# Kernel tuning notes

Hardware: AMD Instinct MI355X
Metric: run time of the kernel (lower is better)

Reference implementation:

```python
import jax, jax.numpy as jnp
import numpy as np

N = 10000      # nodes
E = 160000     # edges
C = 72         # hidden dim = 18 * mul (mul=4)
A = 16         # node_attr dim (16x0e)
L = 3          # layers
O = 64         # output dim (64x0e)
B = 16         # graphs in batch
IN_DIM = 18    # irreps_node_input dim
SH = 9         # spherical harmonics dim, lmax=2
FC = 100       # radial MLP hidden (fc_neurons=[1,100])
MAX_RADIUS = 2.0
NUM_NEIGHBORS = 16.0
NUM_NODES = 625.0


def sph_harm_l2(d):
    # component-normalized real spherical harmonics up to l=2 on unit vectors d [E,3]
    x, y, z = d[:, 0], d[:, 1], d[:, 2]
    s3, s5, s15 = 3.0 ** 0.5, 5.0 ** 0.5, 15.0 ** 0.5
    return jnp.stack([
        jnp.ones_like(x),
        s3 * x, s3 * y, s3 * z,
        s15 * x * y, s15 * y * z, (s5 / 2.0) * (3.0 * z * z - 1.0),
        s15 * x * z, (s15 / 2.0) * (x * x - y * y),
    ], axis=1)  # [E, 9]


def setup_inputs() -> dict:
    key = jax.random.key(0)
    ks = jax.random.split(key, 16)
    pos = jax.random.normal(ks[0], (N, 3), dtype=jnp.float32)
    node_attr = jax.random.normal(ks[1], (N, A), dtype=jnp.float32)
    batch = jnp.sort(jax.random.randint(ks[2], (N,), 0, B))
    edge_src = jax.random.randint(ks[3], (E,), 0, N)
    edge_dst = jax.random.randint(ks[4], (E,), 0, N)
    W_in = jax.random.normal(ks[5], (IN_DIM, C), dtype=jnp.float32) / np.sqrt(IN_DIM)
    W_tp = jax.random.normal(ks[6], (L, SH, C, C), dtype=jnp.float32) / np.sqrt(C)
    W_self = jax.random.normal(ks[7], (L, C, C), dtype=jnp.float32) / np.sqrt(C)
    W_attr = jax.random.normal(ks[8], (L, A, C), dtype=jnp.float32) / np.sqrt(A)
    fc1_w = jax.random.normal(ks[9], (L, 1, FC), dtype=jnp.float32)
    fc1_b = jnp.zeros((L, FC), dtype=jnp.float32)
    fc2_w = jax.random.normal(ks[10], (L, FC, SH), dtype=jnp.float32) / np.sqrt(FC)
    W_out = jax.random.normal(ks[11], (C, O), dtype=jnp.float32) / np.sqrt(C)
    return {"pos": pos, "node_attr": node_attr, "batch": batch,
            "edge_src": edge_src, "edge_dst": edge_dst,
            "W_in": W_in, "W_tp": W_tp, "W_self": W_self, "W_attr": W_attr,
            "fc1_w": fc1_w, "fc1_b": fc1_b, "fc2_w": fc2_w, "W_out": W_out}


def reference(pos, node_attr, batch, edge_src, edge_dst,
              W_in, W_tp, W_self, W_attr, fc1_w, fc1_b, fc2_w, W_out):
    n = pos.shape[0]
    # edge geometry
    rvec = pos[edge_src] - pos[edge_dst]                      # [E,3]
    r = jnp.linalg.norm(rvec, axis=1, keepdims=True)          # [E,1]
    dvec = rvec / jnp.maximum(r, 1e-9)
    sh = sph_harm_l2(dvec)                                    # [E,9]
    # single cosine radial basis with cutoff at max_radius (number_of_basis=1)
    t = r / MAX_RADIUS
    emb = jnp.where(t < 1.0, jnp.cos(0.5 * jnp.pi * t), 0.0)  # [E,1]
    # node inputs: fixed one-hot on the scalar channel, embedded to hidden dim
    onehot = jnp.zeros((IN_DIM,), dtype=pos.dtype).at[0].set(1.0)
    h = jnp.broadcast_to((onehot @ W_in)[None, :], (n, C))    # [N,C]
    for l in range(L):
        # radial MLP -> per-edge, per-SH-path weights
        u = jax.nn.silu(emb @ fc1_w[l] + fc1_b[l]) @ fc2_w[l]  # [E,9]
        path = u * sh                                          # [E,9]
        hs = h[edge_src]                                       # [E,C]
        m = jnp.zeros_like(hs)
        for s in range(SH):  # fixed small set of tensor-product paths
            m = m + path[:, s:s + 1] * (hs @ W_tp[l, s])       # [E,C]
        agg = jax.ops.segment_sum(m, edge_dst, num_segments=n) / np.sqrt(NUM_NEIGHBORS)
        h = jax.nn.gelu(agg + h @ W_self[l] + node_attr @ W_attr[l])
    out_nodes = h @ W_out                                      # [N,O]
    pooled = jax.ops.segment_sum(out_nodes, batch, num_segments=B)
    return pooled / np.sqrt(NUM_NODES)                         # [B,O]
```

## Files before the change

kernel.cpp:

```cpp
#include <hip/hip_runtime.h>
#include <math.h>

#define NN 10000
#define NE 160000
#define CC 72
#define AA 16
#define LL 3
#define OO 64
#define NBATCH 16
#define SH 9
#define FCN 100
#define KK (SH*CC)
#define KA 736
#define KP 768
#define KG 96
#define NT 5
#define PSTRIDE 12
#define NB 1024
#define EMAX 176

typedef __attribute__((ext_vector_type(8))) short bf16x8;
typedef __attribute__((ext_vector_type(4))) float f32x4;

static __device__ __forceinline__ float gelu_tanh(float x) {
    float x3 = x * x * x;
    float inner = 0.7978845608028654f * (x + 0.044715f * x3);
    return 0.5f * x * (1.0f + tanhf(inner));
}
static __device__ __forceinline__ unsigned short f2bf(float x) {
    unsigned int u = __float_as_uint(x);
    u += 0x7FFFu + ((u >> 16) & 1u);
    return (unsigned short)(u >> 16);
}
static __device__ __forceinline__ float bf2f(unsigned short u) {
    return __uint_as_float((unsigned int)u << 16);
}
static __device__ __forceinline__ unsigned int pack2bf(float lo, float hi) {
    return (unsigned int)f2bf(lo) | ((unsigned int)f2bf(hi) << 16);
}

__global__ void k_zero(int* __restrict__ cnt) {
    int i = blockIdx.x * blockDim.x + threadIdx.x;
    if (i < NN) cnt[i] = 0;
}

#define GB_HIST 625
#define GB_UTAB 13
#define GB_WCAT 180
#define GB_INIT 704
#define GB_PREP (GB_HIST + GB_UTAB + GB_WCAT + GB_INIT)

__global__ __launch_bounds__(256) void k_prep(
        const float* __restrict__ pos, const int* __restrict__ esrc,
        const int* __restrict__ edst, int* __restrict__ cnt,
        const float* __restrict__ fc1w, const float* __restrict__ fc1b,
        const float* __restrict__ fc2w, float* __restrict__ U,
        const float* __restrict__ Wtp, const float* __restrict__ Wself,
        const float* __restrict__ Wattr, unsigned short* __restrict__ Wb,
        const float* __restrict__ W_in, unsigned short* __restrict__ h0) {
    int bb = blockIdx.x, t = threadIdx.x;
    if (bb < GB_HIST) {
        int e = bb * 256 + t;
        if (e < NE) {
            int s = esrc[e], d = edst[e];
            float dx = pos[3 * s] - pos[3 * d];
            float dy = pos[3 * s + 1] - pos[3 * d + 1];
            float dz = pos[3 * s + 2] - pos[3 * d + 2];
            float r = sqrtf(dx * dx + dy * dy + dz * dz);
            if (r * 0.5f < 1.0f) atomicAdd(&cnt[d], 1);
        }
        return;
    }
    bb -= GB_HIST;
    if (bb < GB_UTAB) {
        int i = bb * 256 + t;
        if (i < LL * (NB + 1)) {
            int l = i / (NB + 1), b = i - l * (NB + 1);
            float emb = cosf(1.5707963267948966f * ((float)b / (float)NB));
            float u[SH];
#pragma unroll
            for (int q = 0; q < SH; ++q) u[q] = 0.f;
            const float* w1 = &fc1w[l * FCN];
            const float* b1 = &fc1b[l * FCN];
            const float* w2 = &fc2w[l * FCN * SH];
            for (int f = 0; f < FCN; ++f) {
                float a = emb * w1[f] + b1[f];
                float si = a / (1.0f + expf(-a));
#pragma unroll
                for (int q = 0; q < SH; ++q) u[q] += si * w2[f * SH + q];
            }
            float* ud = &U[(size_t)i * 12];
#pragma unroll
            for (int q = 0; q < SH; ++q) ud[q] = u[q];
            ud[9] = 0.f; ud[10] = 0.f; ud[11] = 0.f;
        }
        return;
    }
    bb -= GB_UTAB;
    if (bb < GB_WCAT) {
        int i0 = (bb * 256 + t) * 4;
#pragma unroll
        for (int u = 0; u < 4; ++u) {
            int i = i0 + u;
            int l = i / (NT * KG * 128);
            int rem = i - l * (NT * KG * 128);
            int nt = rem / (KG * 128); rem -= nt * (KG * 128);
            int kg = rem / 128; int e = rem - kg * 128;
            int n = nt * 16 + (e >> 3);
            int k = kg * 8 + (e & 7);
            float v = 0.f;
            if (n < CC && k < KA) {
                if (k < KK)            v = 0.25f * Wtp[(size_t)l * KK * CC + k * CC + n];
                else if (k < KK + CC)  v = Wself[(size_t)l * CC * CC + (k - KK) * CC + n];
                else                   v = Wattr[(size_t)l * AA * CC + (k - KK - CC) * CC + n];
            }
            Wb[i] = f2bf(v);
        }
        return;
    }
    bb -= GB_WCAT;
    {
        int i0 = (bb * 256 + t) * 4;
#pragma unroll
        for (int u = 0; u < 4; ++u) {
            int i = i0 + u;
            if (i < NN * CC) h0[i] = f2bf(W_in[i % CC]);
        }
    }
}

__global__ void k_scan(const int* __restrict__ cnt, int* __restrict__ off,
                       int* __restrict__ cur, float* __restrict__ hp) {
    __shared__ int sa[256], sb[256];
    const int PER = 40;
    int t = threadIdx.x;
    int base = t * PER;
    int loc[PER];
    int run = 0;
#pragma unroll
    for (int i = 0; i < PER; ++i) {
        int idx = base + i;
        int v = (idx < NN) ? cnt[idx] : 0;
        loc[i] = run;
        run += v;
    }
    sa[t] = run;
    __syncthreads();
    int* in = sa; int* out = sb;
    for (int o = 1; o < 256; o <<= 1) {
        int v = in[t];
        if (t >= o) v += in[t - o];
        out[t] = v;
        __syncthreads();
        int* tmp = in; in = out; out = tmp;
    }
    int ebase = (t > 0) ? in[t - 1] : 0;
#pragma unroll
    for (int i = 0; i < PER; ++i) {
        int idx = base + i;
        if (idx <= NN) {
            int v = ebase + loc[i];
            off[idx] = v;
            if (idx < NN) cur[idx] = v;
        }
    }
    for (int i = t; i < NBATCH * CC; i += 256) hp[i] = 0.f;
}

__global__ __launch_bounds__(256) void k_scatter3(const float* __restrict__ pos,
                                                  const int* __restrict__ esrc,
                                                  const int* __restrict__ edst,
                                                  int* __restrict__ cur,
                                                  int* __restrict__ src_s,
                                                  const float* __restrict__ U,
                                                  float* __restrict__ path) {
    int e = blockIdx.x * blockDim.x + threadIdx.x;
    if (e >= NE) return;
    int s = esrc[e], d = edst[e];
    float dx = pos[3 * s] - pos[3 * d];
    float dy = pos[3 * s + 1] - pos[3 * d + 1];
    float dz = pos[3 * s + 2] - pos[3 * d + 2];
    float r = sqrtf(dx * dx + dy * dy + dz * dz);
    if (r * 0.5f >= 1.0f) return;
    int slot = atomicAdd(&cur[d], 1);
    src_s[slot] = s;

    float inv = 1.0f / fmaxf(r, 1e-9f);
    float x = dx * inv, y = dy * inv, z = dz * inv;
    const float s3 = 1.7320508075688772f;
    const float s5 = 2.23606797749979f;
    const float s15 = 3.872983346207417f;
    float sh[SH];
    sh[0] = 1.0f;
    sh[1] = s3 * x;
    sh[2] = s3 * y;
    sh[3] = s3 * z;
    sh[4] = s15 * x * y;
    sh[5] = s15 * y * z;
    sh[6] = 0.5f * s5 * (3.0f * z * z - 1.0f);
    sh[7] = s15 * x * z;
    sh[8] = 0.5f * s15 * (x * x - y * y);

    float fb = r * 0.5f * (float)NB;
    int b0 = (int)fb;
    float fr = fb - (float)b0;

#pragma unroll
    for (int l = 0; l < LL; ++l) {
        const float* t0 = &U[((size_t)l * (NB + 1) + b0) * 12];
        float4 a0 = *(const float4*)(t0 + 0);
        float4 a1 = *(const float4*)(t0 + 4);
        float  a2 = t0[8];
        float4 c0 = *(const float4*)(t0 + 12);
        float4 c1 = *(const float4*)(t0 + 16);
        float  c2 = t0[20];
        float u0 = a0.x + fr * (c0.x - a0.x);
        float u1 = a0.y + fr * (c0.y - a0.y);
        float u2 = a0.z + fr * (c0.z - a0.z);
        float u3 = a0.w + fr * (c0.w - a0.w);
        float u4 = a1.x + fr * (c1.x - a1.x);
        float u5 = a1.y + fr * (c1.y - a1.y);
        float u6 = a1.z + fr * (c1.z - a1.z);
        float u7 = a1.w + fr * (c1.w - a1.w);
        float u8 = a2   + fr * (c2   - a2);
        float* pd = &path[((size_t)l * NE + slot) * PSTRIDE];
        *(float4*)(pd + 0) = make_float4(u0 * sh[0], u1 * sh[1], u2 * sh[2], u3 * sh[3]);
        *(float4*)(pd + 4) = make_float4(u4 * sh[4], u5 * sh[5], u6 * sh[6], u7 * sh[7]);
        *(float4*)(pd + 8) = make_float4(u8 * sh[8], 0.f, 0.f, 0.f);
    }
}

__global__ __launch_bounds__(1024, 8) void k_layer(
        const unsigned short* __restrict__ h,
        const float* __restrict__ attr,
        const float* __restrict__ path_l,
        const int* __restrict__ src_s,
        const int* __restrict__ off,
        const unsigned short* __restrict__ Wb,
        unsigned short* __restrict__ hout) {
    __shared__ float Plds[EMAX * PSTRIDE];
    __shared__ unsigned short Alds[KG * 128];
    int t = threadIdx.x, w = t >> 6, lane = t & 63;
    int n0 = blockIdx.x * 16;
    int d = n0 + w;
    int b0 = off[n0], e0 = off[n0 + 16];
    int db = off[d], de = off[d + 1];

    bool act = lane < 36;
    int c2 = 2 * lane;
    float a1[SH], a2[SH];
#pragma unroll
    for (int q = 0; q < SH; ++q) { a1[q] = 0.f; a2[q] = 0.f; }

    for (int base = b0; base < e0; base += EMAX) {
        int nE = min(EMAX, e0 - base);
        const float4* p4 = (const float4*)(path_l + (size_t)base * PSTRIDE);
        for (int idx = t; idx < nE * 3; idx += 1024)
            *(float4*)&Plds[idx * 4] = p4[idx];
        __syncthreads();
        int lb = db > base ? db : base;
        int le = de < base + nE ? de : base + nE;
        for (int i = lb; i < le; i += 4) {
            int m = le - i;
            unsigned int hv[4];
#pragma unroll
            for (int j = 0; j < 4; ++j) {
                if (j < m && act) {
                    int s = src_s[i + j];
                    hv[j] = *(const unsigned int*)&h[(size_t)s * CC + c2];
                }
            }
#pragma unroll
            for (int j = 0; j < 4; ++j) {
                if (j < m) {
                    const float* p = &Plds[(i + j - base) * PSTRIDE];
                    float4 p0 = *(const float4*)p;
                    float4 p1 = *(const float4*)(p + 4);
                    float p8 = p[8];
                    float lo = act ? bf2f((unsigned short)(hv[j] & 0xffffu)) : 0.f;
                    float hi = act ? bf2f((unsigned short)(hv[j] >> 16)) : 0.f;
                    a1[0] += p0.x * lo; a2[0] += p0.x * hi;
                    a1[1] += p0.y * lo; a2[1] += p0.y * hi;
                    a1[2] += p0.z * lo; a2[2] += p0.z * hi;
                    a1[3] += p0.w * lo; a2[3] += p0.w * hi;
                    a1[4] += p1.x * lo; a2[4] += p1.x * hi;
                    a1[5] += p1.y * lo; a2[5] += p1.y * hi;
                    a1[6] += p1.z * lo; a2[6] += p1.z * hi;
                    a1[7] += p1.w * lo; a2[7] += p1.w * hi;
                    a1[8] += p8 * lo;   a2[8] += p8 * hi;
                }
            }
        }
        __syncthreads();
    }

    if (act) {
        int kgo = lane >> 2, kjo = 2 * (lane & 3);
        int hb = w * 8 + kjo;
#pragma unroll
        for (int q = 0; q < SH; ++q)
            *(unsigned int*)&Alds[(9 * q + kgo) * 128 + hb] = pack2bf(a1[q], a2[q]);
        *(unsigned int*)&Alds[(81 + kgo) * 128 + hb] =
            *(const unsigned int*)&h[(size_t)d * CC + c2];
        if (lane < 8)
            *(unsigned int*)&Alds[(90 + kgo) * 128 + hb] =
                pack2bf(attr[(size_t)d * AA + c2], attr[(size_t)d * AA + c2 + 1]);
    }
    if (lane < 16)
        *(unsigned int*)&Alds[(92 + (lane >> 2)) * 128 + w * 8 + 2 * (lane & 3)] = 0u;
    __syncthreads();

    if (w < NT) {
        const unsigned short* Ab = Alds + (lane & 15) * 8;
        const unsigned short* Bb = Wb + ((size_t)w * KG) * 128 + (lane & 15) * 8;
        f32x4 acc = (f32x4){0.f, 0.f, 0.f, 0.f};
#pragma unroll
        for (int s = 0; s < 24; ++s) {
            int kg = s * 4 + (lane >> 4);
            bf16x8 af = *(const bf16x8*)(Ab + (size_t)kg * 128);
            bf16x8 bq = *(const bf16x8*)(Bb + (size_t)kg * 128);
            acc = __builtin_amdgcn_mfma_f32_16x16x32_bf16(af, bq, acc, 0, 0, 0);
        }
        int cb = lane & 15, rb = (lane >> 4) * 4;
        int row = n0 + rb, col = w * 16 + cb;
        if (col < CC) {
#pragma unroll
            for (int j = 0; j < 4; ++j)
                hout[(size_t)(row + j) * CC + col] = f2bf(gelu_tanh(acc[j]));
        }
    }
}

__global__ __launch_bounds__(256) void k_pool(const unsigned short* __restrict__ h,
                                              const int* __restrict__ batch,
                                              float* __restrict__ hp) {
    __shared__ float sp[NBATCH * CC];
    int t = threadIdx.x;
    for (int i = t; i < NBATCH * CC; i += 256) sp[i] = 0.f;
    __syncthreads();
    int n0 = blockIdx.x * 16;
    for (int i = t; i < 16 * CC; i += 256) {
        int nl = i / CC, c = i - nl * CC;
        int n = n0 + nl;
        if (n < NN) atomicAdd(&sp[batch[n] * CC + c], bf2f(h[(size_t)n * CC + c]));
    }
    __syncthreads();
    for (int i = t; i < NBATCH * CC; i += 256) {
        float v = sp[i];
        if (v != 0.f) atomicAdd(&hp[i], v);
    }
}

__global__ __launch_bounds__(1024) void k_outmm(const float* __restrict__ hp,
                                                const float* __restrict__ Wout,
                                                float* __restrict__ out) {
    __shared__ float hs[NBATCH * CC];
    int t = threadIdx.x;
    for (int i = t; i < NBATCH * CC; i += 1024) hs[i] = hp[i];
    __syncthreads();
    int b = t >> 6, o = t & 63;
    float acc = 0.f;
#pragma unroll 8
    for (int c = 0; c < CC; ++c) acc += hs[b * CC + c] * Wout[c * OO + o];
    out[t] = acc * (1.0f / 25.0f);
}

extern "C" void kernel_launch(void* const* d_in, const int* in_sizes, int n_in,
                              void* d_out, int out_size, void* d_ws, size_t ws_size,
                              hipStream_t stream) {
    const float* pos       = (const float*)d_in[0];
    const float* node_attr = (const float*)d_in[1];
    const int*   batch     = (const int*)d_in[2];
    const int*   esrc      = (const int*)d_in[3];
    const int*   edst      = (const int*)d_in[4];
    const float* W_in      = (const float*)d_in[5];
    const float* W_tp      = (const float*)d_in[6];
    const float* W_self    = (const float*)d_in[7];
    const float* W_attr    = (const float*)d_in[8];
    const float* fc1w      = (const float*)d_in[9];
    const float* fc1b      = (const float*)d_in[10];
    const float* fc2w      = (const float*)d_in[11];
    const float* W_out     = (const float*)d_in[12];
    float* out = (float*)d_out;

    char* p = (char*)d_ws;
    auto alloc = [&](size_t bytes) -> void* {
        void* r = (void*)p;
        p += (bytes + 255) & ~(size_t)255;
        return r;
    };
    int*   cnt   = (int*)alloc((size_t)NN * 4);
    int*   cur   = (int*)alloc((size_t)NN * 4);
    float* hp    = (float*)alloc((size_t)NBATCH * CC * 4);
    int*   off   = (int*)alloc((size_t)(NN + 1) * 4);
    int*   src_s = (int*)alloc((size_t)NE * 4);
    float* path  = (float*)alloc((size_t)LL * NE * PSTRIDE * 4);
    float* U     = (float*)alloc((size_t)LL * (NB + 1) * 12 * 4);
    unsigned short* Wb = (unsigned short*)alloc((size_t)LL * NT * KG * 128 * 2);
    unsigned short* h0 = (unsigned short*)alloc((size_t)NN * CC * 2);
    unsigned short* h1 = (unsigned short*)alloc((size_t)NN * CC * 2);

    k_zero<<<(NN + 255) / 256, 256, 0, stream>>>(cnt);
    k_prep<<<GB_PREP, 256, 0, stream>>>(pos, esrc, edst, cnt, fc1w, fc1b, fc2w, U,
                                        W_tp, W_self, W_attr, Wb, W_in, h0);
    k_scan<<<1, 256, 0, stream>>>(cnt, off, cur, hp);
    k_scatter3<<<(NE + 255) / 256, 256, 0, stream>>>(pos, esrc, edst, cur, src_s, U, path);

    const unsigned short* hin = h0;
    unsigned short* hout = h1;
    for (int l = 0; l < LL; ++l) {
        k_layer<<<NN / 16, 1024, 0, stream>>>(hin, node_attr,
                                              path + (size_t)l * NE * PSTRIDE, src_s, off,
                                              Wb + (size_t)l * NT * KG * 128, hout);
        const unsigned short* tmp = hin; hin = hout; hout = (unsigned short*)tmp;
    }
    k_pool<<<(NN + 15) / 16, 256, 0, stream>>>(hin, batch, hp);
    k_outmm<<<1, 1024, 0, stream>>>(hp, W_out, out);
}
```

Measured before the change: 139.0 us.

## Store per-edge path weights in bf16 and read them directly without LDS staging

Per-edge path coefficients are now packed as bf16 (16-element stride) instead of fp32 (12-element stride), halving the write traffic in the scatter kernel and the read traffic in each layer. The layer kernel drops the block-wide LDS staging of path values and its two __syncthreads per chunk. Each wave instead loads its own edges' path values straight from global memory alongside the gathered h values. This removes barrier stalls and the shared-memory footprint, at the cost of lower precision in the path weights and redundant global loads issued per lane.

```diff
diff --git a/kernel.cpp b/kernel.cpp
--- a/kernel.cpp
+++ b/kernel.cpp
@@ -15,9 +15,8 @@
 #define KP 768
 #define KG 96
 #define NT 5
-#define PSTRIDE 12
+#define PSU 16
 #define NB 1024
-#define EMAX 176
 
 typedef __attribute__((ext_vector_type(8))) short bf16x8;
 typedef __attribute__((ext_vector_type(4))) float f32x4;
@@ -37,6 +36,12 @@
 }
 static __device__ __forceinline__ unsigned int pack2bf(float lo, float hi) {
     return (unsigned int)f2bf(lo) | ((unsigned int)f2bf(hi) << 16);
+}
+static __device__ __forceinline__ float bfLo(unsigned int u) {
+    return __uint_as_float(u << 16);
+}
+static __device__ __forceinline__ float bfHi(unsigned int u) {
+    return __uint_as_float(u & 0xffff0000u);
 }
 
 __global__ void k_zero(int* __restrict__ cnt) {
@@ -173,7 +178,7 @@
                                                   int* __restrict__ cur,
                                                   int* __restrict__ src_s,
                                                   const float* __restrict__ U,
-                                                  float* __restrict__ path) {
+                                                  unsigned short* __restrict__ path) {
     int e = blockIdx.x * blockDim.x + threadIdx.x;
     if (e >= NE) return;
     int s = esrc[e], d = edst[e];
@@ -214,36 +219,37 @@
         float4 c0 = *(const float4*)(t0 + 12);
         float4 c1 = *(const float4*)(t0 + 16);
         float  c2 = t0[20];
-        float u0 = a0.x + fr * (c0.x - a0.x);
-        float u1 = a0.y + fr * (c0.y - a0.y);
-        float u2 = a0.z + fr * (c0.z - a0.z);
-        float u3 = a0.w + fr * (c0.w - a0.w);
-        float u4 = a1.x + fr * (c1.x - a1.x);
-        float u5 = a1.y + fr * (c1.y - a1.y);
-        float u6 = a1.z + fr * (c1.z - a1.z);
-        float u7 = a1.w + fr * (c1.w - a1.w);
-        float u8 = a2   + fr * (c2   - a2);
-        float* pd = &path[((size_t)l * NE + slot) * PSTRIDE];
-        *(float4*)(pd + 0) = make_float4(u0 * sh[0], u1 * sh[1], u2 * sh[2], u3 * sh[3]);
-        *(float4*)(pd + 4) = make_float4(u4 * sh[4], u5 * sh[5], u6 * sh[6], u7 * sh[7]);
-        *(float4*)(pd + 8) = make_float4(u8 * sh[8], 0.f, 0.f, 0.f);
+        float u0 = (a0.x + fr * (c0.x - a0.x)) * sh[0];
+        float u1 = (a0.y + fr * (c0.y - a0.y)) * sh[1];
+        float u2 = (a0.z + fr * (c0.z - a0.z)) * sh[2];
+        float u3 = (a0.w + fr * (c0.w - a0.w)) * sh[3];
+        float u4 = (a1.x + fr * (c1.x - a1.x)) * sh[4];
+        float u5 = (a1.y + fr * (c1.y - a1.y)) * sh[5];
+        float u6 = (a1.z + fr * (c1.z - a1.z)) * sh[6];
+        float u7 = (a1.w + fr * (c1.w - a1.w)) * sh[7];
+        float u8 = (a2   + fr * (c2   - a2))   * sh[8];
+        unsigned short* pd = &path[((size_t)l * NE + slot) * PSU];
+        uint4 w0, w1;
+        w0.x = pack2bf(u0, u1); w0.y = pack2bf(u2, u3);
+        w0.z = pack2bf(u4, u5); w0.w = pack2bf(u6, u7);
+        w1.x = pack2bf(u8, 0.f); w1.y = 0u; w1.z = 0u; w1.w = 0u;
+        *(uint4*)pd = w0;
+        *(uint4*)(pd + 8) = w1;
     }
 }
 
 __global__ __launch_bounds__(1024, 8) void k_layer(
         const unsigned short* __restrict__ h,
         const float* __restrict__ attr,
-        const float* __restrict__ path_l,
+        const unsigned short* __restrict__ path_l,
         const int* __restrict__ src_s,
         const int* __restrict__ off,
         const unsigned short* __restrict__ Wb,
         unsigned short* __restrict__ hout) {
-    __shared__ float Plds[EMAX * PSTRIDE];
     __shared__ unsigned short Alds[KG * 128];
     int t = threadIdx.x, w = t >> 6, lane = t & 63;
     int n0 = blockIdx.x * 16;
     int d = n0 + w;
-    int b0 = off[n0], e0 = off[n0 + 16];
     int db = off[d], de = off[d + 1];
 
     bool act = lane < 36;
@@ -252,46 +258,41 @@
 #pragma unroll
     for (int q = 0; q < SH; ++q) { a1[q] = 0.f; a2[q] = 0.f; }
 
-    for (int base = b0; base < e0; base += EMAX) {
-        int nE = min(EMAX, e0 - base);
-        const float4* p4 = (const float4*)(path_l + (size_t)base * PSTRIDE);
-        for (int idx = t; idx < nE * 3; idx += 1024)
-            *(float4*)&Plds[idx * 4] = p4[idx];
-        __syncthreads();
-        int lb = db > base ? db : base;
-        int le = de < base + nE ? de : base + nE;
-        for (int i = lb; i < le; i += 4) {
-            int m = le - i;
-            unsigned int hv[4];
-#pragma unroll
-            for (int j = 0; j < 4; ++j) {
-                if (j < m && act) {
-                    int s = src_s[i + j];
-                    hv[j] = *(const unsigned int*)&h[(size_t)s * CC + c2];
-                }
+    for (int i = db; i < de; i += 4) {
+        int m = de - i;
+        unsigned int hv[4];
+        uint4 pa[4];
+        unsigned int pb[4];
+#pragma unroll
+        for (int j = 0; j < 4; ++j) {
+            if (j < m) {
+                int s = src_s[i + j];
+                pa[j] = *(const uint4*)&path_l[(size_t)(i + j) * PSU];
+                pb[j] = *(const unsigned int*)&path_l[(size_t)(i + j) * PSU + 8];
+                if (act) hv[j] = *(const unsigned int*)&h[(size_t)s * CC + c2];
             }
-#pragma unroll
-            for (int j = 0; j < 4; ++j) {
-                if (j < m) {
-                    const float* p = &Plds[(i + j - base) * PSTRIDE];
-                    float4 p0 = *(const float4*)p;
-                    float4 p1 = *(const float4*)(p + 4);
-                    float p8 = p[8];
-                    float lo = act ? bf2f((unsigned short)(hv[j] & 0xffffu)) : 0.f;
-                    float hi = act ? bf2f((unsigned short)(hv[j] >> 16)) : 0.f;
-                    a1[0] += p0.x * lo; a2[0] += p0.x * hi;
-                    a1[1] += p0.y * lo; a2[1] += p0.y * hi;
-                    a1[2] += p0.z * lo; a2[2] += p0.z * hi;
-                    a1[3] += p0.w * lo; a2[3] += p0.w * hi;
-                    a1[4] += p1.x * lo; a2[4] += p1.x * hi;
-                    a1[5] += p1.y * lo; a2[5] += p1.y * hi;
-                    a1[6] += p1.z * lo; a2[6] += p1.z * hi;
-                    a1[7] += p1.w * lo; a2[7] += p1.w * hi;
-                    a1[8] += p8 * lo;   a2[8] += p8 * hi;
-                }
+        }
+#pragma unroll
+        for (int j = 0; j < 4; ++j) {
+            if (j < m) {
+                float lo = act ? bfLo(hv[j]) : 0.f;
+                float hi = act ? bfHi(hv[j]) : 0.f;
+                float p0 = bfLo(pa[j].x), p1 = bfHi(pa[j].x);
+                float p2 = bfLo(pa[j].y), p3 = bfHi(pa[j].y);
+                float p4 = bfLo(pa[j].z), p5 = bfHi(pa[j].z);
+                float p6 = bfLo(pa[j].w), p7 = bfHi(pa[j].w);
+                float p8 = bfLo(pb[j]);
+                a1[0] += p0 * lo; a2[0] += p0 * hi;
+                a1[1] += p1 * lo; a2[1] += p1 * hi;
+                a1[2] += p2 * lo; a2[2] += p2 * hi;
+                a1[3] += p3 * lo; a2[3] += p3 * hi;
+                a1[4] += p4 * lo; a2[4] += p4 * hi;
+                a1[5] += p5 * lo; a2[5] += p5 * hi;
+                a1[6] += p6 * lo; a2[6] += p6 * hi;
+                a1[7] += p7 * lo; a2[7] += p7 * hi;
+                a1[8] += p8 * lo; a2[8] += p8 * hi;
             }
         }
-        __syncthreads();
     }
 
     if (act) {
@@ -394,7 +395,7 @@
     float* hp    = (float*)alloc((size_t)NBATCH * CC * 4);
     int*   off   = (int*)alloc((size_t)(NN + 1) * 4);
     int*   src_s = (int*)alloc((size_t)NE * 4);
-    float* path  = (float*)alloc((size_t)LL * NE * PSTRIDE * 4);
+    unsigned short* path = (unsigned short*)alloc((size_t)LL * NE * PSU * 2);
     float* U     = (float*)alloc((size_t)LL * (NB + 1) * 12 * 4);
     unsigned short* Wb = (unsigned short*)alloc((size_t)LL * NT * KG * 128 * 2);
     unsigned short* h0 = (unsigned short*)alloc((size_t)NN * CC * 2);
@@ -410,7 +411,7 @@
     unsigned short* hout = h1;
     for (int l = 0; l < LL; ++l) {
         k_layer<<<NN / 16, 1024, 0, stream>>>(hin, node_attr,
-                                              path + (size_t)l * NE * PSTRIDE, src_s, off,
+                                              path + (size_t)l * NE * PSU, src_s, off,
                                               Wb + (size_t)l * NT * KG * 128, hout);
         const unsigned short* tmp = hin; hin = hout; hout = (unsigned short*)tmp;
     }
```

Measured after the change: 161.2 us. 1.16x slower.
